# Kernel optimization log

Hardware: AMD Instinct MI355X
Metric: run time of the kernel (lower is better)

The kernel has to match this reference:

```python
import jax, jax.numpy as jnp
import numpy as np

TEMPERATURE = 0.5
EPS = 1e-8  # torch.nn.CosineSimilarity eps


def _l2norm(x):
    # torch cosine sim divides by max(||x||, eps) per vector
    n = jnp.sqrt(jnp.sum(x * x, axis=-1, keepdims=True))
    return x / jnp.maximum(n, EPS)


def setup_inputs() -> dict:
    key = jax.random.key(0)
    ka, kb = jax.random.split(key)
    batch_a = jax.random.normal(ka, (4096, 512), dtype=jnp.float32)
    batch_b = jax.random.normal(kb, (4096, 512), dtype=jnp.float32)
    return {"batch_a": batch_a, "batch_b": batch_b}


def reference(batch_a, batch_b):
    a = _l2norm(batch_a)  # [N, D]
    b = _l2norm(batch_b)
    inv_t = 1.0 / TEMPERATURE
    # cosine similarity via normalize + GEMM (same math as broadcast mul+reduce)
    sim11 = (a @ a.T) * inv_t  # [N, N]
    sim22 = (b @ b.T) * inv_t
    sim12 = (a @ b.T) * inv_t
    n = sim12.shape[-1]
    eye = jnp.eye(n, dtype=bool)
    neg_inf = jnp.float32(-jnp.inf)
    sim11 = jnp.where(eye, neg_inf, sim11)
    sim22 = jnp.where(eye, neg_inf, sim22)
    # logits: [[sim12, sim11], [sim22, sim12^T]] -> [2N, 2N]
    logits = jnp.concatenate(
        [jnp.concatenate([sim12, sim11], axis=-1),
         jnp.concatenate([sim22, sim12.T], axis=-1)],
        axis=-2,
    )
    targets = jnp.arange(2 * n)
    logp = jax.nn.log_softmax(logits, axis=-1)  # stable single pass
    loss = -jnp.mean(logp[jnp.arange(2 * n), targets])
    return loss
```

## Files before the change

### kernel.cpp

```cpp
#include <hip/hip_runtime.h>

#define NR 4096
#define DD 512
#define TWO_N 8192
#define MT 64
#define NTILES 2080
#define CHUNK 260

using f32x4 = __attribute__((ext_vector_type(4))) float;
using i32x8 = __attribute__((ext_vector_type(8))) int;

__global__ __launch_bounds__(256) void ntx_nrm_kernel(const float* __restrict__ A,
                                                      const float* __restrict__ B,
                                                      unsigned char* __restrict__ X8,
                                                      float* __restrict__ d12,
                                                      float* __restrict__ S) {
    const int row = blockIdx.x;
    const int t = threadIdx.x;
    const int lane = t & 63, wid = t >> 6;

    if (t < 2) S[row * 2 + t] = 0.f;

    const float2 av = *(const float2*)(A + row * DD + 2 * t);
    const float2 bv = *(const float2*)(B + row * DD + 2 * t);
    float sa = av.x * av.x + av.y * av.y;
    float sb = bv.x * bv.x + bv.y * bv.y;
#pragma unroll
    for (int o = 32; o; o >>= 1) { sa += __shfl_down(sa, o); sb += __shfl_down(sb, o); }

    __shared__ float red[12];
    if (lane == 0) { red[wid] = sa; red[4 + wid] = sb; }
    __syncthreads();
    const float ta = red[0] + red[1] + red[2] + red[3];
    const float tb = red[4] + red[5] + red[6] + red[7];
    const float ra = 1.f / fmaxf(sqrtf(ta), 1e-8f);
    const float rb = 1.f / fmaxf(sqrtf(tb), 1e-8f);
    const float nax = av.x * ra, nay = av.y * ra;
    const float nbx = bv.x * rb, nby = bv.y * rb;

    const unsigned pa = __builtin_amdgcn_cvt_pk_fp8_f32(nax, nay, 0, false);
    const unsigned pb = __builtin_amdgcn_cvt_pk_fp8_f32(nbx, nby, 0, false);
    *(unsigned short*)(X8 + (size_t)row * DD + 2 * t) = (unsigned short)pa;
    *(unsigned short*)(X8 + (size_t)(NR + row) * DD + 2 * t) = (unsigned short)pb;

    float dt = nax * nbx + nay * nby;
#pragma unroll
    for (int o = 32; o; o >>= 1) dt += __shfl_down(dt, o);
    if (lane == 0) red[8 + wid] = dt;
    __syncthreads();
    if (t == 0) d12[row] = red[8] + red[9] + red[10] + red[11];
}

__global__ __launch_bounds__(256) void ntx_gemm_lse_kernel(const unsigned char* __restrict__ X8,
                                                           float* __restrict__ S) {
    const int bid = blockIdx.x;
    const int sid = (bid & 7) * CHUNK + (bid >> 3);
    int u, v;
    if (sid < 1792) {
        const int s = sid >> 6, loc = sid & 63;
        int U = 0;
        while (7 * (U + 1) - (U + 1) * U / 2 <= s) ++U;
        const int V = U + 1 + (s - (7 * U - U * (U - 1) / 2));
        u = U * 8 + (loc >> 3);
        v = V * 8 + (loc & 7);
    } else {
        const int s2 = sid - 1792;
        const int U = s2 / 36, loc = s2 % 36;
        int lu = 0;
        while ((lu + 1) * 8 - (lu + 1) * lu / 2 <= loc) ++lu;
        const int lv = lu + (loc - (lu * 8 - lu * (lu - 1) / 2));
        u = U * 8 + lu;
        v = U * 8 + lv;
    }
    const bool fixedTile = (u == v);
    const int rowTile = u * 128, colTile = (v ^ 32) * 128;

    __shared__ unsigned char As[2][128 * 128];
    __shared__ unsigned char Bs[2][128 * 128];

    const int t = threadIdx.x;
    const int lane = t & 63, wid = t >> 6;
    const int waveRow = wid >> 1, waveCol = wid & 1;
    const int lr = lane & 15, grp = lane >> 4;
    const int r3 = lr & 7;

    f32x4 acc[4][4] = {};

    const int srow = lane >> 3;
    const int scol = ((lane & 7) ^ srow) * 16;

    auto STAGE = [&](int sel, int kb) {
#pragma unroll
        for (int q = 0; q < 4; ++q) {
            const int ci = wid * 4 + q;
            const int r  = ci * 8 + srow;
            const int lo = ci * 1024 + lane * 16;
            __builtin_amdgcn_global_load_lds(
                (const __attribute__((address_space(1))) unsigned*)(X8 + (size_t)(rowTile + r) * DD + kb + scol),
                (__attribute__((address_space(3))) unsigned*)&As[sel][lo], 16, 0, 0);
            __builtin_amdgcn_global_load_lds(
                (const __attribute__((address_space(1))) unsigned*)(X8 + (size_t)((colTile + r) ^ NR) * DD + kb + scol),
                (__attribute__((address_space(3))) unsigned*)&Bs[sel][lo], 16, 0, 0);
        }
    };

    auto COMPUTE = [&](int sel) {
        i32x8 a8[4], b8[4];
#pragma unroll
        for (int m = 0; m < 4; ++m) {
            const int rb = (waveRow * 64 + m * 16 + lr) * 128;
            const int4 lo = *(const int4*)&As[sel][rb + (((grp * 2 + 0) ^ r3) * 16)];
            const int4 hi = *(const int4*)&As[sel][rb + (((grp * 2 + 1) ^ r3) * 16)];
            a8[m][0] = lo.x; a8[m][1] = lo.y; a8[m][2] = lo.z; a8[m][3] = lo.w;
            a8[m][4] = hi.x; a8[m][5] = hi.y; a8[m][6] = hi.z; a8[m][7] = hi.w;
        }
#pragma unroll
        for (int n = 0; n < 4; ++n) {
            const int rb = (waveCol * 64 + n * 16 + lr) * 128;
            const int4 lo = *(const int4*)&Bs[sel][rb + (((grp * 2 + 0) ^ r3) * 16)];
            const int4 hi = *(const int4*)&Bs[sel][rb + (((grp * 2 + 1) ^ r3) * 16)];
            b8[n][0] = lo.x; b8[n][1] = lo.y; b8[n][2] = lo.z; b8[n][3] = lo.w;
            b8[n][4] = hi.x; b8[n][5] = hi.y; b8[n][6] = hi.z; b8[n][7] = hi.w;
        }
#pragma unroll
        for (int m = 0; m < 4; ++m)
#pragma unroll
            for (int n = 0; n < 4; ++n)
                acc[m][n] = __builtin_amdgcn_mfma_scale_f32_16x16x128_f8f6f4(
                    a8[m], b8[n], acc[m][n], 0 , 0 ,
                    0, 0x7F7F7F7F, 0, 0x7F7F7F7F);
    };

    STAGE(0, 0);
    STAGE(1, 128);
#pragma unroll
    for (int i = 0; i < 4; ++i) {
        const int cur = i & 1;
        if (i < 3) asm volatile("s_waitcnt vmcnt(8)" ::: "memory");
        else       asm volatile("s_waitcnt vmcnt(0)" ::: "memory");
        __builtin_amdgcn_s_barrier();
        COMPUTE(cur);
        if (i < 2) {
            asm volatile("s_waitcnt lgkmcnt(0)" ::: "memory");
            __builtin_amdgcn_s_barrier();
            STAGE(cur, (i + 2) * 128);
        }
    }

#pragma unroll
    for (int m = 0; m < 4; ++m)
#pragma unroll
        for (int n = 0; n < 4; ++n)
#pragma unroll
            for (int reg = 0; reg < 4; ++reg) {
                const int R = rowTile + waveRow * 64 + m * 16 + grp * 4 + reg;
                const int C = colTile + waveCol * 64 + n * 16 + lr;
                const bool masked = fixedTile && (C == (R ^ NR));
                acc[m][n][reg] = masked ? 0.f : __expf(acc[m][n][reg] * 2.0f);
            }

#pragma unroll
    for (int m = 0; m < 4; ++m)
#pragma unroll
        for (int reg = 0; reg < 4; ++reg) {
            float rs = acc[m][0][reg] + acc[m][1][reg] + acc[m][2][reg] + acc[m][3][reg];
            rs += __shfl_xor(rs, 1);
            rs += __shfl_xor(rs, 2);
            rs += __shfl_xor(rs, 4);
            rs += __shfl_xor(rs, 8);
            if (lr == 0) {
                const int R = rowTile + waveRow * 64 + m * 16 + grp * 4 + reg;
                atomicAdd(&S[R], rs);
            }
        }

    if (!fixedTile) {
#pragma unroll
        for (int n = 0; n < 4; ++n) {
            float cs = 0.f;
#pragma unroll
            for (int m = 0; m < 4; ++m)
#pragma unroll
                for (int reg = 0; reg < 4; ++reg)
                    cs += acc[m][n][reg];
            cs += __shfl_xor(cs, 16);
            cs += __shfl_xor(cs, 32);
            if (grp == 0) {
                const int C = colTile + waveCol * 64 + n * 16 + lr;
                atomicAdd(&S[C ^ NR], cs);
            }
        }
    }
}

__global__ __launch_bounds__(256) void ntx_loss_kernel(const float* __restrict__ S,
                                                       const float* __restrict__ d12,
                                                       float* __restrict__ out) {
    const int t = threadIdx.x;
    const int r = blockIdx.x * 256 + t;
    float a = __logf(S[r]) - 2.0f * d12[r & (NR - 1)];
    const int lane = t & 63, wid = t >> 6;
#pragma unroll
    for (int o = 32; o; o >>= 1) a += __shfl_down(a, o);
    __shared__ float red[4];
    if (lane == 0) red[wid] = a;
    __syncthreads();
    if (t == 0) atomicAdd(out, (red[0] + red[1] + red[2] + red[3]) * (1.f / (float)TWO_N));
}

extern "C" void kernel_launch(void* const* d_in, const int* in_sizes, int n_in,
                              void* d_out, int out_size, void* d_ws, size_t ws_size,
                              hipStream_t stream) {
    const float* A = (const float*)d_in[0];
    const float* B = (const float*)d_in[1];

    unsigned char* X8 = (unsigned char*)d_ws;
    float* S   = (float*)((char*)d_ws + (size_t)TWO_N * DD);
    float* d12 = (float*)((char*)S + (size_t)TWO_N * 4);

    (void)hipMemsetAsync(d_out, 0, sizeof(float), stream);

    ntx_nrm_kernel<<<NR, 256, 0, stream>>>(A, B, X8, d12, S);

    ntx_gemm_lse_kernel<<<NTILES, 256, 0, stream>>>(X8, S);

    ntx_loss_kernel<<<TWO_N / 256, 256, 0, stream>>>(S, d12, (float*)d_out);
}
```

Baseline: 80.58 us.

## Load full K extent into LDS at once instead of double-buffered pipeline

Replaces the two-stage double-buffered K pipeline with one bulk issue of all four K slices into LDS (128KB total), followed by a single wait and barrier, then four compute steps with no further syncs. This removes the intermediate barriers and waits and lets all global loads be in flight together. In exchange LDS per block grows from 64KB to 128KB, which cuts how many blocks can be resident per CU, and no compute overlaps the loads.

```diff
diff --git a/kernel.cpp b/kernel.cpp
--- a/kernel.cpp
+++ b/kernel.cpp
@@ -75,8 +75,8 @@
     const bool fixedTile = (u == v);
     const int rowTile = u * 128, colTile = (v ^ 32) * 128;
 
-    __shared__ unsigned char As[2][128 * 128];
-    __shared__ unsigned char Bs[2][128 * 128];
+    __shared__ unsigned char As[4 * 128 * 128];
+    __shared__ unsigned char Bs[4 * 128 * 128];
 
     const int t = threadIdx.x;
     const int lane = t & 63, wid = t >> 6;
@@ -89,36 +89,40 @@
     const int srow = lane >> 3;
     const int scol = ((lane & 7) ^ srow) * 16;
 
-    auto STAGE = [&](int sel, int kb) {
+#pragma unroll
+    for (int kb = 0; kb < 4; ++kb) {
 #pragma unroll
         for (int q = 0; q < 4; ++q) {
             const int ci = wid * 4 + q;
             const int r  = ci * 8 + srow;
-            const int lo = ci * 1024 + lane * 16;
+            const int lo = kb * 16384 + ci * 1024 + lane * 16;
             __builtin_amdgcn_global_load_lds(
-                (const __attribute__((address_space(1))) unsigned*)(X8 + (size_t)(rowTile + r) * DD + kb + scol),
-                (__attribute__((address_space(3))) unsigned*)&As[sel][lo], 16, 0, 0);
+                (const __attribute__((address_space(1))) unsigned*)(X8 + (size_t)(rowTile + r) * DD + kb * 128 + scol),
+                (__attribute__((address_space(3))) unsigned*)&As[lo], 16, 0, 0);
             __builtin_amdgcn_global_load_lds(
-                (const __attribute__((address_space(1))) unsigned*)(X8 + (size_t)((colTile + r) ^ NR) * DD + kb + scol),
-                (__attribute__((address_space(3))) unsigned*)&Bs[sel][lo], 16, 0, 0);
-        }
-    };
-
-    auto COMPUTE = [&](int sel) {
+                (const __attribute__((address_space(1))) unsigned*)(X8 + (size_t)((colTile + r) ^ NR) * DD + kb * 128 + scol),
+                (__attribute__((address_space(3))) unsigned*)&Bs[lo], 16, 0, 0);
+        }
+    }
+    asm volatile("s_waitcnt vmcnt(0)" ::: "memory");
+    __builtin_amdgcn_s_barrier();
+
+#pragma unroll
+    for (int kt = 0; kt < 4; ++kt) {
         i32x8 a8[4], b8[4];
 #pragma unroll
         for (int m = 0; m < 4; ++m) {
-            const int rb = (waveRow * 64 + m * 16 + lr) * 128;
-            const int4 lo = *(const int4*)&As[sel][rb + (((grp * 2 + 0) ^ r3) * 16)];
-            const int4 hi = *(const int4*)&As[sel][rb + (((grp * 2 + 1) ^ r3) * 16)];
+            const int rb = kt * 16384 + (waveRow * 64 + m * 16 + lr) * 128;
+            const int4 lo = *(const int4*)&As[rb + (((grp * 2 + 0) ^ r3) * 16)];
+            const int4 hi = *(const int4*)&As[rb + (((grp * 2 + 1) ^ r3) * 16)];
             a8[m][0] = lo.x; a8[m][1] = lo.y; a8[m][2] = lo.z; a8[m][3] = lo.w;
             a8[m][4] = hi.x; a8[m][5] = hi.y; a8[m][6] = hi.z; a8[m][7] = hi.w;
         }
 #pragma unroll
         for (int n = 0; n < 4; ++n) {
-            const int rb = (waveCol * 64 + n * 16 + lr) * 128;
-            const int4 lo = *(const int4*)&Bs[sel][rb + (((grp * 2 + 0) ^ r3) * 16)];
-            const int4 hi = *(const int4*)&Bs[sel][rb + (((grp * 2 + 1) ^ r3) * 16)];
+            const int rb = kt * 16384 + (waveCol * 64 + n * 16 + lr) * 128;
+            const int4 lo = *(const int4*)&Bs[rb + (((grp * 2 + 0) ^ r3) * 16)];
+            const int4 hi = *(const int4*)&Bs[rb + (((grp * 2 + 1) ^ r3) * 16)];
             b8[n][0] = lo.x; b8[n][1] = lo.y; b8[n][2] = lo.z; b8[n][3] = lo.w;
             b8[n][4] = hi.x; b8[n][5] = hi.y; b8[n][6] = hi.z; b8[n][7] = hi.w;
         }
@@ -129,22 +133,6 @@
                 acc[m][n] = __builtin_amdgcn_mfma_scale_f32_16x16x128_f8f6f4(
                     a8[m], b8[n], acc[m][n], 0 , 0 ,
                     0, 0x7F7F7F7F, 0, 0x7F7F7F7F);
-    };
-
-    STAGE(0, 0);
-    STAGE(1, 128);
-#pragma unroll
-    for (int i = 0; i < 4; ++i) {
-        const int cur = i & 1;
-        if (i < 3) asm volatile("s_waitcnt vmcnt(8)" ::: "memory");
-        else       asm volatile("s_waitcnt vmcnt(0)" ::: "memory");
-        __builtin_amdgcn_s_barrier();
-        COMPUTE(cur);
-        if (i < 2) {
-            asm volatile("s_waitcnt lgkmcnt(0)" ::: "memory");
-            __builtin_amdgcn_s_barrier();
-            STAGE(cur, (i + 2) * 128);
-        }
     }
 
 #pragma unroll
```

Result: faster. 77.15 us (median of 2 runs) (-4.3%).

## Replace atomic row-sum accumulation with per-tile partial buffer and deterministic reduction

Applied to the files above, without the earlier changes.

The GEMM kernel now writes each tile's row and column exp-sums into a dedicated slot of a partial-sum buffer indexed by tile-row and diagonal offset, instead of issuing global atomicAdds into S. The loss kernel then sums 128 partials per row before taking the log. This removes atomic contention and the S zeroing in the norm kernel. In exchange the loss kernel reads about 4 MB of partials with a strided access pattern, and the reduction becomes deterministic.

```diff
diff --git a/kernel.cpp b/kernel.cpp
--- a/kernel.cpp
+++ b/kernel.cpp
@@ -13,13 +13,10 @@
 __global__ __launch_bounds__(256) void ntx_nrm_kernel(const float* __restrict__ A,
                                                       const float* __restrict__ B,
                                                       unsigned char* __restrict__ X8,
-                                                      float* __restrict__ d12,
-                                                      float* __restrict__ S) {
+                                                      float* __restrict__ d12) {
     const int row = blockIdx.x;
     const int t = threadIdx.x;
     const int lane = t & 63, wid = t >> 6;
-
-    if (t < 2) S[row * 2 + t] = 0.f;
 
     const float2 av = *(const float2*)(A + row * DD + 2 * t);
     const float2 bv = *(const float2*)(B + row * DD + 2 * t);
@@ -52,7 +49,7 @@
 }
 
 __global__ __launch_bounds__(256) void ntx_gemm_lse_kernel(const unsigned char* __restrict__ X8,
-                                                           float* __restrict__ S) {
+                                                           float* __restrict__ P) {
     const int bid = blockIdx.x;
     const int sid = (bid & 7) * CHUNK + (bid >> 3);
     int u, v;
@@ -159,6 +156,7 @@
                 acc[m][n][reg] = masked ? 0.f : __expf(acc[m][n][reg] * 2.0f);
             }
 
+    const int dslot = v - u;
 #pragma unroll
     for (int m = 0; m < 4; ++m)
 #pragma unroll
@@ -169,8 +167,8 @@
             rs += __shfl_xor(rs, 4);
             rs += __shfl_xor(rs, 8);
             if (lr == 0) {
-                const int R = rowTile + waveRow * 64 + m * 16 + grp * 4 + reg;
-                atomicAdd(&S[R], rs);
+                const int roff = waveRow * 64 + m * 16 + grp * 4 + reg;
+                P[(((size_t)u * 64 + dslot) * 2 + waveCol) * 128 + roff] = rs;
             }
         }
 
@@ -186,19 +184,24 @@
             cs += __shfl_xor(cs, 16);
             cs += __shfl_xor(cs, 32);
             if (grp == 0) {
-                const int C = colTile + waveCol * 64 + n * 16 + lr;
-                atomicAdd(&S[C ^ NR], cs);
+                const int coff = waveCol * 64 + n * 16 + lr;
+                P[(((size_t)v * 64 + (64 - dslot)) * 2 + waveRow) * 128 + coff] = cs;
             }
         }
     }
 }
 
-__global__ __launch_bounds__(256) void ntx_loss_kernel(const float* __restrict__ S,
+__global__ __launch_bounds__(256) void ntx_loss_kernel(const float* __restrict__ P,
                                                        const float* __restrict__ d12,
                                                        float* __restrict__ out) {
     const int t = threadIdx.x;
     const int r = blockIdx.x * 256 + t;
-    float a = __logf(S[r]) - 2.0f * d12[r & (NR - 1)];
+    const float* Pr = P + (size_t)(r >> 7) * 64 * 2 * 128 + (r & 127);
+    float sum = 0.f;
+#pragma unroll 8
+    for (int s = 0; s < 128; ++s)
+        sum += Pr[(size_t)s * 128];
+    float a = __logf(sum) - 2.0f * d12[r & (NR - 1)];
     const int lane = t & 63, wid = t >> 6;
 #pragma unroll
     for (int o = 32; o; o >>= 1) a += __shfl_down(a, o);
@@ -215,14 +218,14 @@
     const float* B = (const float*)d_in[1];
 
     unsigned char* X8 = (unsigned char*)d_ws;
-    float* S   = (float*)((char*)d_ws + (size_t)TWO_N * DD);
-    float* d12 = (float*)((char*)S + (size_t)TWO_N * 4);
+    float* d12 = (float*)((char*)d_ws + (size_t)TWO_N * DD);
+    float* P   = (float*)((char*)d12 + (size_t)NR * 4);
 
     (void)hipMemsetAsync(d_out, 0, sizeof(float), stream);
 
-    ntx_nrm_kernel<<<NR, 256, 0, stream>>>(A, B, X8, d12, S);
-
-    ntx_gemm_lse_kernel<<<NTILES, 256, 0, stream>>>(X8, S);
-
-    ntx_loss_kernel<<<TWO_N / 256, 256, 0, stream>>>(S, d12, (float*)d_out);
-}
+    ntx_nrm_kernel<<<NR, 256, 0, stream>>>(A, B, X8, d12);
+
+    ntx_gemm_lse_kernel<<<NTILES, 256, 0, stream>>>(X8, P);
+
+    ntx_loss_kernel<<<TWO_N / 256, 256, 0, stream>>>(P, d12, (float*)d_out);
+}
```

Measured after the change: 84.99 us. 5.5% more time.
